# Kernel tuning notes

Hardware: AMD Instinct MI355X
Metric: run time of the kernel (lower is better)

The kernel has to match this reference:

```python
import jax, jax.numpy as jnp
import numpy as np

IN_FEATURES = 256
N_HEADS = 4
N_HIDDEN = 128  # out_features, concat=False
SLOPE = 0.1
NEG_INF = -9e15


def setup_inputs() -> dict:
    key = jax.random.key(0)
    k1, k2, k3, k4 = jax.random.split(key, 4)
    N = 8192
    h = jax.random.normal(k1, (N, IN_FEATURES), dtype=jnp.float32)
    adj_mat = jax.random.randint(k2, (N, N), 0, 2, dtype=jnp.int32)
    # xavier_normal with gain=1.414
    std_W = 1.414 * (2.0 / (IN_FEATURES + N_HIDDEN * N_HEADS)) ** 0.5
    W = jax.random.normal(k3, (IN_FEATURES, N_HIDDEN * N_HEADS), dtype=jnp.float32) * std_W
    std_a = 1.414 * (2.0 / (2 * N_HIDDEN + 1)) ** 0.5
    a = jax.random.normal(k4, (N_HEADS, 2 * N_HIDDEN, 1), dtype=jnp.float32) * std_a
    return {"h": h, "adj_mat": adj_mat, "W": W, "a": a}


def reference(h, adj_mat, W, a):
    N = h.shape[0]
    # linear projection -> [H, N, d]
    ht = (h @ W).reshape(N, N_HEADS, N_HIDDEN).transpose(1, 0, 2)
    # dropout is identity (eval / p effectively 0), then LeakyReLU
    ht = jnp.where(ht >= 0, ht, SLOPE * ht)
    # additive attention scores: src[h,i] + tgt[h,j]
    src = jnp.einsum('hnd,hd->hn', ht, a[:, :N_HIDDEN, 0])  # [H, N]
    tgt = jnp.einsum('hnd,hd->hn', ht, a[:, N_HIDDEN:, 0])  # [H, N]
    e = src[:, :, None] + tgt[:, None, :]                   # [H, N, N]
    e = jnp.where(adj_mat[None, :, :] > 0, e, NEG_INF)
    attn = jax.nn.softmax(e, axis=-1)
    # weighted sum and mean over heads (concat=False)
    out = jnp.einsum('hnm,hmd->hnd', attn, ht).mean(axis=0)  # [N, d]
    return out
```

## Files before the change

kernel.cpp:

```cpp
#include <hip/hip_runtime.h>


typedef unsigned short u16;
typedef unsigned int u32;
using bf16x8 = __attribute__((ext_vector_type(8))) short;
using f32x4  = __attribute__((ext_vector_type(4))) float;
using i32x4  = __attribute__((ext_vector_type(4))) int;

__device__ __forceinline__ u16 f2bf(float f) {
  u32 u = __float_as_uint(f);
  return (u16)((u + 0x7FFFu + ((u >> 16) & 1u)) >> 16);
}
__device__ __forceinline__ float bf2f(u16 u) {
  return __uint_as_float(((u32)u) << 16);
}

__global__ void pack_adj(const int* __restrict__ adj, u32* __restrict__ adjb) {
  int idx = blockIdx.x * 256 + threadIdx.x;
  const int* p = adj + (size_t)idx * 32;
  u32 m = 0;
#pragma unroll
  for (int c = 0; c < 8; ++c) {
    i32x4 v = __builtin_nontemporal_load((const i32x4*)(p + 4 * c));
    m |= (v[0] != 0 ? 1u : 0u) << (4 * c);
    m |= (v[1] != 0 ? 1u : 0u) << (4 * c + 1);
    m |= (v[2] != 0 ? 1u : 0u) << (4 * c + 2);
    m |= (v[3] != 0 ? 1u : 0u) << (4 * c + 3);
  }
  adjb[idx] = m;
}

__global__ void transpose_w(const float* __restrict__ W, float* __restrict__ Wt) {
  __shared__ float tile[32][33];
  int cb = blockIdx.x * 32, kb = blockIdx.y * 32;
  int tc = threadIdx.x & 31, tr = threadIdx.x >> 5;
  for (int p = 0; p < 32; p += 8)
    tile[tr + p][tc] = W[(size_t)(kb + tr + p) * 512 + cb + tc];
  __syncthreads();
  for (int p = 0; p < 32; p += 8)
    Wt[(size_t)(cb + tr + p) * 256 + kb + tc] = tile[tc][tr + p];
}

__global__ void ht_gemm(const float* __restrict__ h, const float* __restrict__ Wt,
                        u16* __restrict__ HT) {
  __shared__ __align__(16) u16 Abuf[128 * 40];
  __shared__ __align__(16) u16 Bbuf[128 * 40];
  int tid = threadIdx.x;
  int cb = blockIdx.x, rb = blockIdx.y;
  int r0 = rb * 128, c0 = cb * 128;
  int lane = tid & 63, wv = tid >> 6;
  int wr = wv >> 1, wc = wv & 1;
  int mrow = lane & 15, q = lane >> 4;
  int ch = tid & 7, m0 = tid >> 3;

  f32x4 acc[4][4];
#pragma unroll
  for (int i = 0; i < 4; i++)
#pragma unroll
    for (int j = 0; j < 4; j++) acc[i][j] = f32x4{0.f, 0.f, 0.f, 0.f};

  for (int kt = 0; kt < 256; kt += 32) {
    __syncthreads();
#pragma unroll
    for (int mp = 0; mp < 128; mp += 32) {
      int m = m0 + mp;
      float4 v = *(const float4*)(&h[(size_t)(r0 + m) * 256 + kt + ch * 4]);
      uint2 p;
      p.x = (u32)f2bf(v.x) | ((u32)f2bf(v.y) << 16);
      p.y = (u32)f2bf(v.z) | ((u32)f2bf(v.w) << 16);
      *(uint2*)(&Abuf[m * 40 + ch * 4]) = p;
      float4 u = *(const float4*)(&Wt[(size_t)(c0 + m) * 256 + kt + ch * 4]);
      uint2 r;
      r.x = (u32)f2bf(u.x) | ((u32)f2bf(u.y) << 16);
      r.y = (u32)f2bf(u.z) | ((u32)f2bf(u.w) << 16);
      *(uint2*)(&Bbuf[m * 40 + ch * 4]) = r;
    }
    __syncthreads();
    bf16x8 af[4], bfv[4];
#pragma unroll
    for (int i = 0; i < 4; i++)
      af[i] = *(const bf16x8*)(&Abuf[(wr * 64 + i * 16 + mrow) * 40 + q * 8]);
#pragma unroll
    for (int j = 0; j < 4; j++)
      bfv[j] = *(const bf16x8*)(&Bbuf[(wc * 64 + j * 16 + mrow) * 40 + q * 8]);
#pragma unroll
    for (int i = 0; i < 4; i++)
#pragma unroll
      for (int j = 0; j < 4; j++)
        acc[i][j] = __builtin_amdgcn_mfma_f32_16x16x32_bf16(af[i], bfv[j], acc[i][j], 0, 0, 0);
  }
#pragma unroll
  for (int i = 0; i < 4; i++)
#pragma unroll
    for (int j = 0; j < 4; j++)
#pragma unroll
      for (int r = 0; r < 4; r++) {
        int gi = r0 + wr * 64 + i * 16 + q * 4 + r;
        int gc = c0 + wc * 64 + j * 16 + mrow;
        float v = acc[i][j][r];
        v = v >= 0.f ? v : 0.1f * v;
        HT[(size_t)gi * 512 + gc] = f2bf(v);
      }
}

__global__ void build_yt(const u16* __restrict__ HT, const float* __restrict__ a,
                         u16* __restrict__ Yt) {
  __shared__ u16 sht[32][528];
  __shared__ float swv[32 * 4];
  __shared__ float sa[512];
  int t = threadIdx.x;
  int j0 = blockIdx.x * 32;
  for (int i = t; i < 512; i += 256) {
    int g = i >> 7, d = i & 127;
    sa[i] = a[g * 256 + 128 + d];
  }
#pragma unroll
  for (int p = 0; p < 8; ++p) {
    int el = t + 256 * p;
    int row = el >> 6, col8 = el & 63;
    *(uint4*)(&sht[row][col8 * 8]) = *(const uint4*)(&HT[(size_t)(j0 + row) * 512 + col8 * 8]);
  }
  __syncthreads();
  if (t < 128) {
    int jl = t >> 2, g = t & 3;
    float acc = 0.f;
#pragma unroll
    for (int d8 = 0; d8 < 16; ++d8) {
      bf16x8 v = *(const bf16x8*)(&sht[jl][g * 128 + d8 * 8]);
#pragma unroll
      for (int u = 0; u < 8; ++u)
        acc += bf2f((u16)v[u]) * sa[g * 128 + d8 * 8 + u];
    }
    swv[jl * 4 + g] = __expf(acc);
  }
  __syncthreads();
  int oj = (t & 3) * 8, oc = t >> 2;
  size_t T = j0 >> 5;
  for (int pass = 0; pass < 9; ++pass) {
    int c = pass * 64 + oc;
    if (c >= 528) break;
    u32 pk[4] = {0u, 0u, 0u, 0u};
    if (c < 512) {
      int g = c >> 7;
#pragma unroll
      for (int u = 0; u < 4; ++u) {
        int j = oj + 2 * u;
        float v0 = bf2f(sht[j][c]) * swv[j * 4 + g];
        float v1 = bf2f(sht[j + 1][c]) * swv[(j + 1) * 4 + g];
        pk[u] = (u32)f2bf(v0) | ((u32)f2bf(v1) << 16);
      }
    } else if (c < 516) {
      int g = c - 512;
#pragma unroll
      for (int u = 0; u < 4; ++u) {
        int j = oj + 2 * u;
        float v0 = swv[j * 4 + g];
        float v1 = swv[(j + 1) * 4 + g];
        pk[u] = (u32)f2bf(v0) | ((u32)f2bf(v1) << 16);
      }
    }
    size_t dst = ((size_t)(c >> 4) * 256 + T) * 512 + (size_t)(oj >> 3) * 128 + (c & 15) * 8;
    *(uint4*)(&Yt[dst]) = make_uint4(pk[0], pk[1], pk[2], pk[3]);
  }
}

__global__ __launch_bounds__(512) void adj_gemm(const u32* __restrict__ adjb,
                                                const u16* __restrict__ Yt,
                                                float* __restrict__ C,
                                                float* __restrict__ S) {
  int tid = threadIdx.x;
  int rb = blockIdx.y, kh = blockIdx.x;
  int r0 = rb * 128;
  int w0 = kh * 64;
  int lane = tid & 63, wv = tid >> 6;
  int wr = wv >> 2, wc = wv & 3;
  int mrow = lane & 15, q = lane >> 4;
  u32 sh = q * 8;
  bool do_den = (wc == 0);
  const u32* mbase = adjb + (size_t)(r0 + wr * 64 + mrow) * 256 + w0;
  const u16* ybase = Yt + ((size_t)(wc * 8) * 256 + (size_t)w0) * 512 + (size_t)lane * 8;
  const u16* dbase = Yt + ((size_t)32 * 256 + (size_t)w0) * 512 + (size_t)lane * 8;

  f32x4 acc[4][8];
#pragma unroll
  for (int i = 0; i < 4; i++)
#pragma unroll
    for (int j = 0; j < 8; j++) acc[i][j] = f32x4{0.f, 0.f, 0.f, 0.f};
  f32x4 accD[4];
#pragma unroll
  for (int i = 0; i < 4; i++) accD[i] = f32x4{0.f, 0.f, 0.f, 0.f};

  for (int t = 0; t < 64; ++t) {
    bf16x8 bfv[8];
#pragma unroll
    for (int j = 0; j < 8; j++)
      bfv[j] = *(const bf16x8*)(ybase + ((size_t)j * 256 + t) * 512);
    bf16x8 bd;
    if (do_den) bd = *(const bf16x8*)(dbase + (size_t)t * 512);
    bf16x8 af[4];
#pragma unroll
    for (int i = 0; i < 4; i++) {
      u32 m = mbase[(size_t)i * 4096 + t];
      u32 b = (m >> sh) & 0xFFu;
      u32 w[4];
#pragma unroll
      for (int e = 0; e < 4; ++e)
        w[e] = (((b >> (2 * e)) & 1u) ? 0x3F80u : 0u) |
               (((b >> (2 * e + 1)) & 1u) ? 0x3F800000u : 0u);
      af[i] = *(const bf16x8*)&w[0];
    }
    __builtin_amdgcn_s_setprio(1);
#pragma unroll
    for (int j = 0; j < 8; j++)
#pragma unroll
      for (int i = 0; i < 4; i++)
        acc[i][j] = __builtin_amdgcn_mfma_f32_16x16x32_bf16(af[i], bfv[j], acc[i][j], 0, 0, 0);
    if (do_den) {
#pragma unroll
      for (int i = 0; i < 4; i++)
        accD[i] = __builtin_amdgcn_mfma_f32_16x16x32_bf16(af[i], bd, accD[i], 0, 0, 0);
    }
    __builtin_amdgcn_s_setprio(0);
  }

  float* Ck = C + (size_t)kh * 8192 * 512;
#pragma unroll
  for (int i = 0; i < 4; i++)
#pragma unroll
    for (int j = 0; j < 8; j++)
#pragma unroll
      for (int r = 0; r < 4; r++) {
        int gi = r0 + wr * 64 + i * 16 + q * 4 + r;
        int gc = wc * 128 + j * 16 + mrow;
        Ck[(size_t)gi * 512 + gc] = acc[i][j][r];
      }
  if (do_den && mrow < 4) {
    float* Sk = S + (size_t)kh * 4 * 8192;
#pragma unroll
    for (int i = 0; i < 4; i++)
#pragma unroll
      for (int r = 0; r < 4; r++) {
        int gi = r0 + wr * 64 + i * 16 + q * 4 + r;
        Sk[(size_t)mrow * 8192 + gi] = accD[i][r];
      }
  }
}

__global__ void finalize_gat(const float* __restrict__ C, const float* __restrict__ S,
                             float* __restrict__ out) {
  int idx = blockIdx.x * 256 + threadIdx.x;
  int i = idx >> 7, d = idx & 127;
  float s = 0.f;
#pragma unroll
  for (int g = 0; g < 4; ++g) {
    float num = 0.f, den = 0.f;
#pragma unroll
    for (int kh = 0; kh < 4; ++kh) {
      num += C[(size_t)kh * 8192 * 512 + (size_t)i * 512 + g * 128 + d];
      den += S[(size_t)kh * 4 * 8192 + (size_t)g * 8192 + i];
    }
    s += num / den;
  }
  out[idx] = 0.25f * s;
}

extern "C" void kernel_launch(void* const* d_in, const int* in_sizes, int n_in,
                              void* d_out, int out_size, void* d_ws, size_t ws_size,
                              hipStream_t stream) {
  const float* h   = (const float*)d_in[0];
  const int*   adj = (const int*)d_in[1];
  const float* W   = (const float*)d_in[2];
  const float* a   = (const float*)d_in[3];
  float* out = (float*)d_out;
  char* ws = (char*)d_ws;
  float* Wt = (float*)(ws + 0);
  u16*   HT = (u16*)(ws + 524288);
  u16*   Yt = (u16*)(ws + 8912896);
  float* C  = (float*)(ws + 17563648);
  float* S  = (float*)(ws + 84672512);
  u32*  adjb = (u32*)(ws + 84803584);

  pack_adj<<<dim3(8192), 256, 0, stream>>>(adj, adjb);
  transpose_w<<<dim3(16, 8), 256, 0, stream>>>(W, Wt);
  ht_gemm<<<dim3(4, 64), 256, 0, stream>>>(h, Wt, HT);
  build_yt<<<dim3(256), 256, 0, stream>>>(HT, a, Yt);
  adj_gemm<<<dim3(4, 64), 512, 0, stream>>>(adjb, Yt, C, S);
  finalize_gat<<<dim3(4096), 256, 0, stream>>>(C, S, out);
}
```

Before: 552.4 us.

## Stage adj_gemm operands through LDS with async triple-buffered loads

```diff
diff --git a/kernel.cpp b/kernel.cpp
--- a/kernel.cpp
+++ b/kernel.cpp
@@ -6,6 +6,10 @@
 using bf16x8 = __attribute__((ext_vector_type(8))) short;
 using f32x4  = __attribute__((ext_vector_type(4))) float;
 using i32x4  = __attribute__((ext_vector_type(4))) int;
+
+typedef const void __attribute__((address_space(1))) gas_void;
+typedef void __attribute__((address_space(3))) las_void;
+#define GLD16(g, l) __builtin_amdgcn_global_load_lds((gas_void*)(g), (las_void*)(l), 16, 0, 0)
 
 __device__ __forceinline__ u16 f2bf(float f) {
   u32 u = __float_as_uint(f);
@@ -135,7 +139,6 @@
   }
   __syncthreads();
   int oj = (t & 3) * 8, oc = t >> 2;
-  size_t T = j0 >> 5;
   for (int pass = 0; pass < 9; ++pass) {
     int c = pass * 64 + oc;
     if (c >= 528) break;
@@ -159,27 +162,33 @@
         pk[u] = (u32)f2bf(v0) | ((u32)f2bf(v1) << 16);
       }
     }
-    size_t dst = ((size_t)(c >> 4) * 256 + T) * 512 + (size_t)(oj >> 3) * 128 + (c & 15) * 8;
-    *(uint4*)(&Yt[dst]) = make_uint4(pk[0], pk[1], pk[2], pk[3]);
-  }
-}
-
-__global__ __launch_bounds__(512) void adj_gemm(const u32* __restrict__ adjb,
-                                                const u16* __restrict__ Yt,
-                                                float* __restrict__ C,
-                                                float* __restrict__ S) {
+    *(uint4*)(&Yt[(size_t)c * 8192 + j0 + oj]) = make_uint4(pk[0], pk[1], pk[2], pk[3]);
+  }
+}
+
+__global__ __launch_bounds__(256, 2) void adj_gemm(const u32* __restrict__ adjb,
+                                                   const u16* __restrict__ Yt,
+                                                   float* __restrict__ C,
+                                                   float* __restrict__ S) {
+  __shared__ __align__(16) u16 Bbuf[3][272 * 32];
+  __shared__ __align__(16) u16 Abuf[2][128 * 32];
   int tid = threadIdx.x;
-  int rb = blockIdx.y, kh = blockIdx.x;
-  int r0 = rb * 128;
-  int w0 = kh * 64;
+  int bx = blockIdx.x, rb = blockIdx.y;
+  int kh = bx & 3, cs = bx >> 2;
+  int r0 = rb * 128, k0 = kh * 2048, w0 = kh * 64;
   int lane = tid & 63, wv = tid >> 6;
-  int wr = wv >> 2, wc = wv & 3;
+  int wr = wv >> 1, wc = wv & 1;
   int mrow = lane & 15, q = lane >> 4;
-  u32 sh = q * 8;
-  bool do_den = (wc == 0);
-  const u32* mbase = adjb + (size_t)(r0 + wr * 64 + mrow) * 256 + w0;
-  const u16* ybase = Yt + ((size_t)(wc * 8) * 256 + (size_t)w0) * 512 + (size_t)lane * 8;
-  const u16* dbase = Yt + ((size_t)32 * 256 + (size_t)w0) * 512 + (size_t)lane * 8;
+  int qs = q ^ ((mrow >> 1) & 3);
+  int am = tid >> 1, ah = tid & 1;
+  int arx = (am >> 1) & 3;
+  int as0 = am * 32 + ((ah * 2) ^ arx) * 8;
+  int as1 = am * 32 + ((ah * 2 + 1) ^ arx) * 8;
+  const u32* ab = adjb + (size_t)(r0 + am) * 256 + w0;
+  int brow = lane >> 2;
+  int bq = (lane & 3) ^ ((lane >> 3) & 3);
+  bool den_stage = (cs == 0 && wv == 0);
+  bool den_mfma  = (cs == 0 && wc == 0);
 
   f32x4 acc[4][8];
 #pragma unroll
@@ -190,38 +199,88 @@
 #pragma unroll
   for (int i = 0; i < 4; i++) accD[i] = f32x4{0.f, 0.f, 0.f, 0.f};
 
+#define EXPANDA(DST, M)                                                      \
+  {                                                                          \
+    u32 hh = ((M) >> (ah * 16)) & 0xFFFFu;                                   \
+    u32 b0 = hh & 0xFFu, b1 = hh >> 8;                                       \
+    uint4 p0, p1;                                                            \
+    p0.x = ((b0 & 1u) ? 0x3F80u : 0u) | ((b0 & 2u) ? 0x3F800000u : 0u);      \
+    p0.y = ((b0 & 4u) ? 0x3F80u : 0u) | ((b0 & 8u) ? 0x3F800000u : 0u);      \
+    p0.z = ((b0 & 16u) ? 0x3F80u : 0u) | ((b0 & 32u) ? 0x3F800000u : 0u);    \
+    p0.w = ((b0 & 64u) ? 0x3F80u : 0u) | ((b0 & 128u) ? 0x3F800000u : 0u);   \
+    p1.x = ((b1 & 1u) ? 0x3F80u : 0u) | ((b1 & 2u) ? 0x3F800000u : 0u);      \
+    p1.y = ((b1 & 4u) ? 0x3F80u : 0u) | ((b1 & 8u) ? 0x3F800000u : 0u);      \
+    p1.z = ((b1 & 16u) ? 0x3F80u : 0u) | ((b1 & 32u) ? 0x3F800000u : 0u);    \
+    p1.w = ((b1 & 64u) ? 0x3F80u : 0u) | ((b1 & 128u) ? 0x3F800000u : 0u);   \
+    *(uint4*)((DST) + as0) = p0;                                             \
+    *(uint4*)((DST) + as1) = p1;                                             \
+  }
+#define STAGE_B(DB, KT)                                                      \
+  {                                                                          \
+    _Pragma("unroll") for (int p = 0; p < 4; ++p)                            \
+        GLD16(&Yt[(size_t)(cs * 256 + (wv + 4 * p) * 16 + brow) * 8192 + (KT) + bq * 8], \
+              (DB) + ((wv + 4 * p) * 16) * 32);                              \
+    if (den_stage)                                                           \
+      GLD16(&Yt[(size_t)(512 + brow) * 8192 + (KT) + bq * 8], (DB) + 256 * 32); \
+  }
+#define WAIT_KEEP()                                                          \
+  {                                                                          \
+    if (den_stage) asm volatile("s_waitcnt vmcnt(5)" ::: "memory");          \
+    else           asm volatile("s_waitcnt vmcnt(4)" ::: "memory");          \
+  }
+
+  {
+    u32 m0 = ab[0];
+    STAGE_B(&Bbuf[0][0], k0);
+    STAGE_B(&Bbuf[1][0], k0 + 32);
+    EXPANDA(&Abuf[0][0], m0);
+    WAIT_KEEP();
+    asm volatile("s_waitcnt lgkmcnt(0)" ::: "memory");
+    __builtin_amdgcn_s_barrier();
+  }
+
+  u16 *bcur = &Bbuf[0][0], *bnxt = &Bbuf[1][0], *bnn = &Bbuf[2][0];
+
   for (int t = 0; t < 64; ++t) {
-    bf16x8 bfv[8];
+    u32 m;
+    if (t < 63) m = ab[t + 1];
+    if (t < 62) STAGE_B(bnn, k0 + (t + 2) * 32);
+    bf16x8 af[4], bfv[8];
+    const u16* Ab = &Abuf[t & 1][0];
+#pragma unroll
+    for (int i = 0; i < 4; i++)
+      af[i] = *(const bf16x8*)(&Ab[(wr * 64 + i * 16 + mrow) * 32 + qs * 8]);
 #pragma unroll
     for (int j = 0; j < 8; j++)
-      bfv[j] = *(const bf16x8*)(ybase + ((size_t)j * 256 + t) * 512);
-    bf16x8 bd;
-    if (do_den) bd = *(const bf16x8*)(dbase + (size_t)t * 512);
-    bf16x8 af[4];
-#pragma unroll
-    for (int i = 0; i < 4; i++) {
-      u32 m = mbase[(size_t)i * 4096 + t];
-      u32 b = (m >> sh) & 0xFFu;
-      u32 w[4];
-#pragma unroll
-      for (int e = 0; e < 4; ++e)
-        w[e] = (((b >> (2 * e)) & 1u) ? 0x3F80u : 0u) |
-               (((b >> (2 * e + 1)) & 1u) ? 0x3F800000u : 0u);
-      af[i] = *(const bf16x8*)&w[0];
-    }
+      bfv[j] = *(const bf16x8*)(&bcur[((wc * 8 + j) * 16 + mrow) * 32 + qs * 8]);
     __builtin_amdgcn_s_setprio(1);
 #pragma unroll
-    for (int j = 0; j < 8; j++)
-#pragma unroll
-      for (int i = 0; i < 4; i++)
+    for (int i = 0; i < 4; i++)
+#pragma unroll
+      for (int j = 0; j < 8; j++)
         acc[i][j] = __builtin_amdgcn_mfma_f32_16x16x32_bf16(af[i], bfv[j], acc[i][j], 0, 0, 0);
-    if (do_den) {
+    if (den_mfma) {
+      bf16x8 bd = *(const bf16x8*)(&bcur[(256 + mrow) * 32 + qs * 8]);
 #pragma unroll
       for (int i = 0; i < 4; i++)
         accD[i] = __builtin_amdgcn_mfma_f32_16x16x32_bf16(af[i], bd, accD[i], 0, 0, 0);
     }
     __builtin_amdgcn_s_setprio(0);
-  }
+    if (t < 63) EXPANDA(&Abuf[(t + 1) & 1][0], m);
+    if (t < 62) {
+      WAIT_KEEP();
+    } else if (t == 62) {
+      asm volatile("s_waitcnt vmcnt(0)" ::: "memory");
+    }
+    if (t < 63) {
+      asm volatile("s_waitcnt lgkmcnt(0)" ::: "memory");
+      __builtin_amdgcn_s_barrier();
+    }
+    u16* tb = bcur; bcur = bnxt; bnxt = bnn; bnn = tb;
+  }
+#undef EXPANDA
+#undef STAGE_B
+#undef WAIT_KEEP
 
   float* Ck = C + (size_t)kh * 8192 * 512;
 #pragma unroll
@@ -231,10 +290,10 @@
 #pragma unroll
       for (int r = 0; r < 4; r++) {
         int gi = r0 + wr * 64 + i * 16 + q * 4 + r;
-        int gc = wc * 128 + j * 16 + mrow;
+        int gc = cs * 256 + wc * 128 + j * 16 + mrow;
         Ck[(size_t)gi * 512 + gc] = acc[i][j][r];
       }
-  if (do_den && mrow < 4) {
+  if (den_mfma && mrow < 4) {
     float* Sk = S + (size_t)kh * 4 * 8192;
 #pragma unroll
     for (int i = 0; i < 4; i++)
@@ -284,6 +343,6 @@
   transpose_w<<<dim3(16, 8), 256, 0, stream>>>(W, Wt);
   ht_gemm<<<dim3(4, 64), 256, 0, stream>>>(h, Wt, HT);
   build_yt<<<dim3(256), 256, 0, stream>>>(HT, a, Yt);
-  adj_gemm<<<dim3(4, 64), 512, 0, stream>>>(adjb, Yt, C, S);
+  adj_gemm<<<dim3(8, 64), 256, 0, stream>>>(adjb, Yt, C, S);
   finalize_gat<<<dim3(4096), 256, 0, stream>>>(C, S, out);
 }
```

Measured after the change: 521.4 us. -5.6%, faster.
